# Optimization experiments

Measured on AMD Instinct MI355X. Metric: run time of the kernel, lower is better.

The kernel has to match this reference:

```python
import jax, jax.numpy as jnp
import numpy as np

N_NODES = 50000
N_EDGES = 800000
IN_DIM = 64
HID_DIM = 128
OUT_DIM = 64
BN_EPS = 1e-5


def _glorot(key, shape):
    fan_in, fan_out = shape[0], shape[1]
    lim = (6.0 / (fan_in + fan_out)) ** 0.5
    return jax.random.uniform(key, shape, jnp.float32, -lim, lim)


def setup_inputs() -> dict:
    key = jax.random.key(0)
    ks = jax.random.split(key, 8)
    x = jax.random.normal(ks[0], (N_NODES, IN_DIM), jnp.float32)
    edge_index = jax.random.randint(ks[1], (2, N_EDGES), 0, N_NODES, jnp.int32)
    return {
        "x": x,
        "edge_index": edge_index,
        # SAGEConv1: lin_l (applied to aggregated neighbors, has bias), lin_r (root, no bias)
        "W1l": _glorot(ks[2], (IN_DIM, HID_DIM)),
        "b1": jnp.zeros((HID_DIM,), jnp.float32),
        "W1r": _glorot(ks[3], (IN_DIM, HID_DIM)),
        # BatchNorm1d params
        "gamma": jnp.ones((HID_DIM,), jnp.float32),
        "beta": jnp.zeros((HID_DIM,), jnp.float32),
        # SAGEConv2
        "W2l": _glorot(ks[4], (HID_DIM, OUT_DIM)),
        "b2": jnp.zeros((OUT_DIM,), jnp.float32),
        "W2r": _glorot(ks[5], (HID_DIM, OUT_DIM)),
    }


def _sage_conv(h, src, dst, Wl, b, Wr, deg_inv):
    # mean-aggregate neighbor features per destination node
    agg = jax.ops.segment_sum(h[src], dst, num_segments=N_NODES)  # [N, d]
    agg = agg * deg_inv[:, None]
    return agg @ Wl + b + h @ Wr


def reference(x, edge_index, W1l, b1, W1r, gamma, beta, W2l, b2, W2r):
    src, dst = edge_index[0], edge_index[1]
    deg = jax.ops.segment_sum(jnp.ones((N_EDGES,), jnp.float32), dst,
                              num_segments=N_NODES)
    deg_inv = jnp.where(deg > 0, 1.0 / jnp.maximum(deg, 1.0), 0.0)

    h = _sage_conv(x, src, dst, W1l, b1, W1r, deg_inv)  # [N, hid]
    # BatchNorm1d (training mode: batch stats over nodes, biased variance)
    mu = jnp.mean(h, axis=0)
    var = jnp.mean((h - mu) ** 2, axis=0)
    h = (h - mu) * jax.lax.rsqrt(var + BN_EPS) * gamma + beta
    h = jax.nn.relu(h)
    out = _sage_conv(h, src, dst, W2l, b2, W2r, deg_inv)  # [N, out]
    return out
```

## Files before the change

kernel.cpp:

```cpp
#include <hip/hip_runtime.h>

#define NN 50000
#define NE 800000
#define HID 128
#define OUTD 64
#define NBK 782
#define BWID 64
#define CAP 1264
#define TILE_E 4096
#define XB 3125
#define HB 196

typedef __attribute__((ext_vector_type(8))) short bf16x8;
typedef __attribute__((ext_vector_type(4))) float f32x4;

static __device__ __forceinline__ unsigned short f2bf(float f) {
    unsigned u = __float_as_uint(f);
    unsigned r = (u + 0x7FFFu + ((u >> 16) & 1u)) >> 16;
    return (unsigned short)r;
}
static __device__ __forceinline__ float bflo(unsigned u) { return __uint_as_float(u << 16); }
static __device__ __forceinline__ float bfhi(unsigned u) { return __uint_as_float(u & 0xffff0000u); }

__global__ __launch_bounds__(256) void prep_bin_kernel(
    const float* __restrict__ x, unsigned short* __restrict__ xb,
    const float* __restrict__ W1l, const float* __restrict__ W1r,
    const float* __restrict__ W2l, const float* __restrict__ W2r,
    unsigned short* __restrict__ BT1, unsigned short* __restrict__ BT2,
    const int* __restrict__ src, const int* __restrict__ dst,
    int* __restrict__ gcur, unsigned* __restrict__ pairs)
{
    __shared__ int lcnt[NBK];
    __shared__ int lbase[NBK];
    int blk = blockIdx.x, tid = threadIdx.x;
    if (blk >= HB) {
        int b2 = blk - HB;
        if (b2 < XB) {
            int idx = b2 * 256 + tid;
            int n = idx >> 4, q = idx & 15;
            float4 v = ((const float4*)x)[idx];
            ushort4 o;
            o.x = f2bf(v.x); o.y = f2bf(v.y); o.z = f2bf(v.z); o.w = f2bf(v.w);
            *(ushort4*)(xb + (size_t)n * 64 + q * 4) = o;
        } else {
            int idx = (b2 - XB) * 256 + tid;
            int j = idx >> 7, k = idx & 127;
            float v1 = (k < 64) ? W1l[k * HID + j] : W1r[(k - 64) * HID + j];
            BT1[j * 128 + k] = f2bf(v1);
            float v2 = (j < 64) ? W2l[k * OUTD + j] : W2r[k * OUTD + (j - 64)];
            BT2[j * 128 + k] = f2bf(v2);
        }
        return;
    }
    int e0 = blk * TILE_E;
    for (int i = tid; i < NBK; i += 256) lcnt[i] = 0;
    __syncthreads();
    int s[16], d[16], loc[16];
#pragma unroll
    for (int i = 0; i < 16; i++) {
        int e = e0 + i * 256 + tid;
        if (e < NE) {
            s[i] = __builtin_nontemporal_load(&src[e]);
            d[i] = __builtin_nontemporal_load(&dst[e]);
            loc[i] = atomicAdd(&lcnt[d[i] >> 6], 1);
        }
    }
    __syncthreads();
    for (int b = tid; b < NBK; b += 256)
        lbase[b] = b * CAP + atomicAdd(&gcur[b], lcnt[b]);
    __syncthreads();
#pragma unroll
    for (int i = 0; i < 16; i++) {
        int e = e0 + i * 256 + tid;
        if (e < NE)
            pairs[lbase[d[i] >> 6] + loc[i]] =
                (unsigned)(((d[i] & 63) << 16) | s[i]);
    }
}

__global__ __launch_bounds__(256) void agg_conv1_kernel(
    const unsigned* __restrict__ pairs, const int* __restrict__ gcur,
    const unsigned short* __restrict__ xb, const unsigned short* __restrict__ BT,
    const float* __restrict__ bias, unsigned short* __restrict__ hpreb,
    float* __restrict__ sums, float* __restrict__ sumsq,
    unsigned short* __restrict__ permG, unsigned short* __restrict__ degG,
    unsigned short* __restrict__ startG)
{
    __shared__ int lcnt[BWID];
    __shared__ int startL[BWID];
    __shared__ int degL[BWID];
    __shared__ int lcur[BWID];
    __shared__ __align__(16) unsigned short permL[CAP];
    __shared__ __align__(16) unsigned short aggL[64][64];
    __shared__ float red_s[4][128];
    __shared__ float red_q[4][128];
    int b = blockIdx.x, tid = threadIdx.x;
    int lo = b * CAP;
    int cnt = gcur[b];
    if (tid < BWID) lcnt[tid] = 0;
    __syncthreads();
    for (int i = tid; i < cnt; i += 256)
        atomicAdd(&lcnt[pairs[lo + i] >> 16], 1);
    __syncthreads();
    if (tid < BWID) {
        int v = lcnt[tid];
        int s = v;
#pragma unroll
        for (int off = 1; off < BWID; off <<= 1) {
            int t = __shfl_up(s, off, 64);
            if (tid >= off) s += t;
        }
        startL[tid] = s - v;
        degL[tid] = v;
        lcur[tid] = s - v;
        degG[b * 64 + tid] = (unsigned short)v;
        startG[b * 64 + tid] = (unsigned short)(s - v);
    }
    __syncthreads();
    for (int i = tid; i < cnt; i += 256) {
        unsigned p = pairs[lo + i];
        int pos = atomicAdd(&lcur[p >> 16], 1);
        permL[pos] = (unsigned short)(p & 0xffffu);
    }
    __syncthreads();
    int cu = (cnt + 1) >> 1;
    for (int i = tid; i < cu; i += 256)
        ((unsigned*)(permG + lo))[i] = ((const unsigned*)permL)[i];
    int lane = tid & 63, w = tid >> 6;
    int g = lane >> 3;
    int q = lane & 7;
    const unsigned short* fbase = xb + q * 8;
#pragma unroll
    for (int rnd = 0; rnd < 2; rnd++) {
        int nloc = w * 16 + rnd * 8 + g;
        int rs = startL[nloc];
        int deg = degL[nloc];
        float acc[8];
#pragma unroll
        for (int t = 0; t < 8; t++) acc[t] = 0.f;
        int i = 0;
        for (; i + 3 < deg; i += 4) {
            int s0 = permL[rs + i];
            int s1 = permL[rs + i + 1];
            int s2 = permL[rs + i + 2];
            int s3 = permL[rs + i + 3];
            uint4 v0 = *(const uint4*)(fbase + (size_t)s0 * 64);
            uint4 v1 = *(const uint4*)(fbase + (size_t)s1 * 64);
            uint4 v2 = *(const uint4*)(fbase + (size_t)s2 * 64);
            uint4 v3 = *(const uint4*)(fbase + (size_t)s3 * 64);
            acc[0] += bflo(v0.x); acc[1] += bfhi(v0.x);
            acc[2] += bflo(v0.y); acc[3] += bfhi(v0.y);
            acc[4] += bflo(v0.z); acc[5] += bfhi(v0.z);
            acc[6] += bflo(v0.w); acc[7] += bfhi(v0.w);
            acc[0] += bflo(v1.x); acc[1] += bfhi(v1.x);
            acc[2] += bflo(v1.y); acc[3] += bfhi(v1.y);
            acc[4] += bflo(v1.z); acc[5] += bfhi(v1.z);
            acc[6] += bflo(v1.w); acc[7] += bfhi(v1.w);
            acc[0] += bflo(v2.x); acc[1] += bfhi(v2.x);
            acc[2] += bflo(v2.y); acc[3] += bfhi(v2.y);
            acc[4] += bflo(v2.z); acc[5] += bfhi(v2.z);
            acc[6] += bflo(v2.w); acc[7] += bfhi(v2.w);
            acc[0] += bflo(v3.x); acc[1] += bfhi(v3.x);
            acc[2] += bflo(v3.y); acc[3] += bfhi(v3.y);
            acc[4] += bflo(v3.z); acc[5] += bfhi(v3.z);
            acc[6] += bflo(v3.w); acc[7] += bfhi(v3.w);
        }
        for (; i < deg; i++) {
            int s0 = permL[rs + i];
            uint4 v0 = *(const uint4*)(fbase + (size_t)s0 * 64);
            acc[0] += bflo(v0.x); acc[1] += bfhi(v0.x);
            acc[2] += bflo(v0.y); acc[3] += bfhi(v0.y);
            acc[4] += bflo(v0.z); acc[5] += bfhi(v0.z);
            acc[6] += bflo(v0.w); acc[7] += bfhi(v0.w);
        }
        float inv = (deg > 0) ? (1.0f / (float)deg) : 0.f;
        uint4 o;
        o.x = (unsigned)f2bf(acc[0] * inv) | ((unsigned)f2bf(acc[1] * inv) << 16);
        o.y = (unsigned)f2bf(acc[2] * inv) | ((unsigned)f2bf(acc[3] * inv) << 16);
        o.z = (unsigned)f2bf(acc[4] * inv) | ((unsigned)f2bf(acc[5] * inv) << 16);
        o.w = (unsigned)f2bf(acc[6] * inv) | ((unsigned)f2bf(acc[7] * inv) << 16);
        *(uint4*)&aggL[nloc][q * 8] = o;
    }
    __syncthreads();
    int nl = lane & 15, ko = lane >> 4;
    int jh = w & 1;
    bf16x8 bfr[4][4];
    const unsigned short* bbase = BT + (size_t)(jh * 64 + nl) * 128 + ko * 8;
#pragma unroll
    for (int jg = 0; jg < 4; jg++)
#pragma unroll
        for (int ks = 0; ks < 4; ks++)
            bfr[jg][ks] = *(const bf16x8*)(bbase + jg * 16 * 128 + ks * 32);
    float4 bias4[4];
#pragma unroll
    for (int jg = 0; jg < 4; jg++)
        bias4[jg] = *(const float4*)(bias + jh * 64 + jg * 16 + ko * 4);
    float s_sum[16], s_sq[16];
#pragma unroll
    for (int t = 0; t < 16; t++) { s_sum[t] = 0.f; s_sq[t] = 0.f; }
#pragma unroll
    for (int rnd2 = 0; rnd2 < 2; rnd2++) {
        int t = (w >> 1) + rnd2 * 2;
        int n_g = b * 64 + t * 16 + nl;
        if (n_g < NN) {
            bf16x8 a[4];
#pragma unroll
            for (int ks = 0; ks < 2; ks++)
                a[ks] = *(const bf16x8*)&aggL[t * 16 + nl][ks * 32 + ko * 8];
            const unsigned short* xrow = xb + (size_t)n_g * 64 + ko * 8;
#pragma unroll
            for (int ks = 2; ks < 4; ks++)
                a[ks] = *(const bf16x8*)(xrow + (ks - 2) * 32);
#pragma unroll
            for (int jg = 0; jg < 4; jg++) {
                f32x4 acc = {0.f, 0.f, 0.f, 0.f};
#pragma unroll
                for (int ks = 0; ks < 4; ks++)
                    acc = __builtin_amdgcn_mfma_f32_16x16x32_bf16(bfr[jg][ks], a[ks], acc, 0, 0, 0);
                float v0 = acc[0] + bias4[jg].x;
                float v1 = acc[1] + bias4[jg].y;
                float v2 = acc[2] + bias4[jg].z;
                float v3 = acc[3] + bias4[jg].w;
                s_sum[jg * 4 + 0] += v0; s_sq[jg * 4 + 0] += v0 * v0;
                s_sum[jg * 4 + 1] += v1; s_sq[jg * 4 + 1] += v1 * v1;
                s_sum[jg * 4 + 2] += v2; s_sq[jg * 4 + 2] += v2 * v2;
                s_sum[jg * 4 + 3] += v3; s_sq[jg * 4 + 3] += v3 * v3;
                uint2 pk;
                pk.x = (unsigned)f2bf(v0) | ((unsigned)f2bf(v1) << 16);
                pk.y = (unsigned)f2bf(v2) | ((unsigned)f2bf(v3) << 16);
                *(uint2*)(hpreb + (size_t)n_g * 128 + jh * 64 + jg * 16 + ko * 4) = pk;
            }
        }
    }
    for (int i = tid; i < 512; i += 256) {
        ((float*)red_s)[i] = 0.f;
        ((float*)red_q)[i] = 0.f;
    }
    __syncthreads();
#pragma unroll
    for (int jg = 0; jg < 4; jg++) {
#pragma unroll
        for (int r = 0; r < 4; r++) {
            float v = s_sum[jg * 4 + r];
            v += __shfl_xor(v, 1, 64);
            v += __shfl_xor(v, 2, 64);
            v += __shfl_xor(v, 4, 64);
            v += __shfl_xor(v, 8, 64);
            float w2 = s_sq[jg * 4 + r];
            w2 += __shfl_xor(w2, 1, 64);
            w2 += __shfl_xor(w2, 2, 64);
            w2 += __shfl_xor(w2, 4, 64);
            w2 += __shfl_xor(w2, 8, 64);
            if (nl == 0) {
                red_s[w][jh * 64 + jg * 16 + ko * 4 + r] = v;
                red_q[w][jh * 64 + jg * 16 + ko * 4 + r] = w2;
            }
        }
    }
    __syncthreads();
    if (tid < 128) {
        float v = red_s[0][tid] + red_s[1][tid] + red_s[2][tid] + red_s[3][tid];
        atomicAdd(&sums[tid], v);
    } else {
        int j = tid - 128;
        float v = red_q[0][j] + red_q[1][j] + red_q[2][j] + red_q[3][j];
        atomicAdd(&sumsq[j], v);
    }
}

static __device__ __forceinline__ bf16x8 bnrelu8(uint4 v, const float* sc,
                                                 const float* sh, int j0) {
    float f[8];
    f[0] = bflo(v.x); f[1] = bfhi(v.x);
    f[2] = bflo(v.y); f[3] = bfhi(v.y);
    f[4] = bflo(v.z); f[5] = bfhi(v.z);
    f[6] = bflo(v.w); f[7] = bfhi(v.w);
#pragma unroll
    for (int t = 0; t < 8; t++) {
        float h = f[t] * sc[j0 + t] + sh[j0 + t];
        f[t] = h > 0.f ? h : 0.f;
    }
    unsigned r01 = (unsigned)f2bf(f[0]) | ((unsigned)f2bf(f[1]) << 16);
    unsigned r23 = (unsigned)f2bf(f[2]) | ((unsigned)f2bf(f[3]) << 16);
    unsigned r45 = (unsigned)f2bf(f[4]) | ((unsigned)f2bf(f[5]) << 16);
    unsigned r67 = (unsigned)f2bf(f[6]) | ((unsigned)f2bf(f[7]) << 16);
    uint4 o = make_uint4(r01, r23, r45, r67);
    return *(bf16x8*)&o;
}

__global__ __launch_bounds__(256) void conv2_kernel(
    const unsigned short* __restrict__ A, const unsigned short* __restrict__ BT,
    const float* __restrict__ bias,
    unsigned short* __restrict__ pb, float* __restrict__ outf,
    const float* __restrict__ sums, const float* __restrict__ sumsq,
    const float* __restrict__ gamma, const float* __restrict__ beta)
{
    __shared__ float sc[128], sh[128];
    int tid = threadIdx.x;
    int wid = tid >> 6, lane = tid & 63;
    int nl = lane & 15, ko = lane >> 4;
    if (tid < 128) {
        float inv_n = 1.0f / (float)NN;
        float mu = sums[tid] * inv_n;
        float var = sumsq[tid] * inv_n - mu * mu;
        float s = gamma[tid] * rsqrtf(var + 1e-5f);
        sc[tid] = s;
        sh[tid] = beta[tid] - mu * s;
    }
    __syncthreads();
    int gw = blockIdx.x * 4 + wid;
    int jh = gw & 1;
    int tstride = (gridDim.x * 4) >> 1;
    const int tiles = NN / 16;
    bf16x8 bfr[4][4];
    const unsigned short* bbase = BT + (size_t)(jh * 64 + nl) * 128 + ko * 8;
#pragma unroll
    for (int jg = 0; jg < 4; jg++)
#pragma unroll
        for (int ks = 0; ks < 4; ks++)
            bfr[jg][ks] = *(const bf16x8*)(bbase + jg * 16 * 128 + ks * 32);
    float4 bias4[4];
#pragma unroll
    for (int jg = 0; jg < 4; jg++) {
        if (jh) bias4[jg] = *(const float4*)(bias + jg * 16 + ko * 4);
        else    bias4[jg] = make_float4(0.f, 0.f, 0.f, 0.f);
    }
    int tile = gw >> 1;
    uint4 a[4];
    if (tile < tiles) {
        const unsigned short* arow = A + (size_t)(tile * 16 + nl) * 128 + ko * 8;
#pragma unroll
        for (int ks = 0; ks < 4; ks++) a[ks] = *(const uint4*)(arow + ks * 32);
    }
    while (tile < tiles) {
        int nxt = tile + tstride;
        uint4 an[4];
        if (nxt < tiles) {
            const unsigned short* arow = A + (size_t)(nxt * 16 + nl) * 128 + ko * 8;
#pragma unroll
            for (int ks = 0; ks < 4; ks++) an[ks] = *(const uint4*)(arow + ks * 32);
        }
        bf16x8 af[4];
#pragma unroll
        for (int ks = 0; ks < 4; ks++)
            af[ks] = bnrelu8(a[ks], sc, sh, ks * 32 + ko * 8);
        int n_g = tile * 16 + nl;
#pragma unroll
        for (int jg = 0; jg < 4; jg++) {
            f32x4 acc = {0.f, 0.f, 0.f, 0.f};
#pragma unroll
            for (int ks = 0; ks < 4; ks++)
                acc = __builtin_amdgcn_mfma_f32_16x16x32_bf16(bfr[jg][ks], af[ks], acc, 0, 0, 0);
            float v0 = acc[0] + bias4[jg].x;
            float v1 = acc[1] + bias4[jg].y;
            float v2 = acc[2] + bias4[jg].z;
            float v3 = acc[3] + bias4[jg].w;
            if (jh == 0) {
                uint2 pk;
                pk.x = (unsigned)f2bf(v0) | ((unsigned)f2bf(v1) << 16);
                pk.y = (unsigned)f2bf(v2) | ((unsigned)f2bf(v3) << 16);
                *(uint2*)(pb + (size_t)n_g * 64 + jg * 16 + ko * 4) = pk;
            } else {
                float4 o = make_float4(v0, v1, v2, v3);
                *(float4*)(outf + (size_t)n_g * 64 + jg * 16 + ko * 4) = o;
            }
        }
#pragma unroll
        for (int ks = 0; ks < 4; ks++) a[ks] = an[ks];
        tile = nxt;
    }
}

__global__ __launch_bounds__(256) void agg2_kernel(
    const unsigned short* __restrict__ permG, const int* __restrict__ gcur,
    const unsigned short* __restrict__ degG, const unsigned short* __restrict__ startG,
    const unsigned short* __restrict__ pb, float* __restrict__ out)
{
    __shared__ __align__(16) unsigned short permL[CAP];
    __shared__ int startL[BWID];
    __shared__ int degL[BWID];
    int b = blockIdx.x, tid = threadIdx.x;
    int lo = b * CAP;
    int cnt = gcur[b];
    if (tid < BWID) {
        startL[tid] = startG[b * 64 + tid];
        degL[tid] = degG[b * 64 + tid];
    }
    int cu = (cnt + 1) >> 1;
    for (int i = tid; i < cu; i += 256)
        ((unsigned*)permL)[i] = ((const unsigned*)(permG + lo))[i];
    __syncthreads();
    int lane = tid & 63, w = tid >> 6;
    int g = lane >> 3;
    int q = lane & 7;
    const unsigned short* fbase = pb + q * 8;
#pragma unroll
    for (int rnd = 0; rnd < 2; rnd++) {
        int nloc = w * 16 + rnd * 8 + g;
        int node = b * 64 + nloc;
        int rs = startL[nloc];
        int deg = degL[nloc];
        float acc[8];
#pragma unroll
        for (int t = 0; t < 8; t++) acc[t] = 0.f;
        int i = 0;
        for (; i + 3 < deg; i += 4) {
            int s0 = permL[rs + i];
            int s1 = permL[rs + i + 1];
            int s2 = permL[rs + i + 2];
            int s3 = permL[rs + i + 3];
            uint4 v0 = *(const uint4*)(fbase + (size_t)s0 * 64);
            uint4 v1 = *(const uint4*)(fbase + (size_t)s1 * 64);
            uint4 v2 = *(const uint4*)(fbase + (size_t)s2 * 64);
            uint4 v3 = *(const uint4*)(fbase + (size_t)s3 * 64);
            acc[0] += bflo(v0.x); acc[1] += bfhi(v0.x);
            acc[2] += bflo(v0.y); acc[3] += bfhi(v0.y);
            acc[4] += bflo(v0.z); acc[5] += bfhi(v0.z);
            acc[6] += bflo(v0.w); acc[7] += bfhi(v0.w);
            acc[0] += bflo(v1.x); acc[1] += bfhi(v1.x);
            acc[2] += bflo(v1.y); acc[3] += bfhi(v1.y);
            acc[4] += bflo(v1.z); acc[5] += bfhi(v1.z);
            acc[6] += bflo(v1.w); acc[7] += bfhi(v1.w);
            acc[0] += bflo(v2.x); acc[1] += bfhi(v2.x);
            acc[2] += bflo(v2.y); acc[3] += bfhi(v2.y);
            acc[4] += bflo(v2.z); acc[5] += bfhi(v2.z);
            acc[6] += bflo(v2.w); acc[7] += bfhi(v2.w);
            acc[0] += bflo(v3.x); acc[1] += bfhi(v3.x);
            acc[2] += bflo(v3.y); acc[3] += bfhi(v3.y);
            acc[4] += bflo(v3.z); acc[5] += bfhi(v3.z);
            acc[6] += bflo(v3.w); acc[7] += bfhi(v3.w);
        }
        for (; i < deg; i++) {
            int s0 = permL[rs + i];
            uint4 v0 = *(const uint4*)(fbase + (size_t)s0 * 64);
            acc[0] += bflo(v0.x); acc[1] += bfhi(v0.x);
            acc[2] += bflo(v0.y); acc[3] += bfhi(v0.y);
            acc[4] += bflo(v0.z); acc[5] += bfhi(v0.z);
            acc[6] += bflo(v0.w); acc[7] += bfhi(v0.w);
        }
        if (node < NN) {
            float inv = (deg > 0) ? (1.0f / (float)deg) : 0.f;
            float4* op = (float4*)(out + (size_t)node * 64 + q * 8);
            float4 o0 = op[0], o1 = op[1];
            o0.x += acc[0] * inv; o0.y += acc[1] * inv;
            o0.z += acc[2] * inv; o0.w += acc[3] * inv;
            o1.x += acc[4] * inv; o1.y += acc[5] * inv;
            o1.z += acc[6] * inv; o1.w += acc[7] * inv;
            op[0] = o0; op[1] = o1;
        }
    }
}

extern "C" void kernel_launch(void* const* d_in, const int* in_sizes, int n_in,
                              void* d_out, int out_size, void* d_ws, size_t ws_size,
                              hipStream_t stream) {
    const float* x     = (const float*)d_in[0];
    const int*   ei    = (const int*)d_in[1];
    const float* W1l   = (const float*)d_in[2];
    const float* b1    = (const float*)d_in[3];
    const float* W1r   = (const float*)d_in[4];
    const float* gamma = (const float*)d_in[5];
    const float* beta  = (const float*)d_in[6];
    const float* W2l   = (const float*)d_in[7];
    const float* b2    = (const float*)d_in[8];
    const float* W2r   = (const float*)d_in[9];
    float* out = (float*)d_out;

    char* wsb = (char*)d_ws;
    int*   gcur   = (int*)wsb;
    float* sums   = (float*)(wsb + 4096);
    float* sumsq  = sums + 128;
    unsigned* pairs = (unsigned*)(wsb + 8192);
    unsigned short* permG  = (unsigned short*)((char*)pairs + (size_t)NBK * CAP * 4);
    unsigned short* degG   = permG + (size_t)NBK * CAP;
    unsigned short* startG = degG + (size_t)NBK * 64;
    unsigned short* xb     = startG + (size_t)NBK * 64;
    unsigned short* hpreb  = xb + (size_t)NN * 64;
    unsigned short* pbuf   = hpreb + (size_t)NN * 128;
    unsigned short* BT1    = pbuf + (size_t)NN * 64;
    unsigned short* BT2    = BT1 + 128 * 128;

    const int* srcp = ei;
    const int* dstp = ei + NE;

    hipMemsetAsync(d_ws, 0, 8192, stream);

    prep_bin_kernel<<<HB + XB + 64, 256, 0, stream>>>(x, xb, W1l, W1r, W2l, W2r,
                                                      BT1, BT2, srcp, dstp, gcur, pairs);
    agg_conv1_kernel<<<NBK, 256, 0, stream>>>(pairs, gcur, xb, BT1, b1, hpreb,
                                              sums, sumsq, permG, degG, startG);
    conv2_kernel<<<512, 256, 0, stream>>>(hpreb, BT2, b2, pbuf, out,
                                          sums, sumsq, gamma, beta);
    agg2_kernel<<<NBK, 256, 0, stream>>>(permG, gcur, degG, startG, pbuf, out);
}
```

Baseline: 190.5 us.

## Split each destination bucket across two blocks in both aggregation kernels

Both aggregation kernels now launch two blocks per 64-node destination bucket. Each block handles 32 destination nodes, filtering the bucket's pairs by half, and stores its own permutation slice and count (cntH) for reuse in the second aggregation. The aim is to double block count, giving more parallelism and finer load balance across CUs, and to shrink per-block LDS so more blocks fit per CU. The cost is that each block scans the full bucket's pairs twice. Bucket capacity is enlarged so each half fits in a fixed 704-entry slot, which adds a small overflow risk if one half receives an unusually large share of edges.

Result: no change. 188.0 us (-1.3%).

```diff
diff --git a/kernel.cpp b/kernel.cpp
--- a/kernel.cpp
+++ b/kernel.cpp
@@ -6,7 +6,8 @@
 #define OUTD 64
 #define NBK 782
 #define BWID 64
-#define CAP 1264
+#define CAP 1408
+#define CAPH 704
 #define TILE_E 4096
 #define XB 3125
 #define HB 196
@@ -84,57 +85,68 @@
     const float* __restrict__ bias, unsigned short* __restrict__ hpreb,
     float* __restrict__ sums, float* __restrict__ sumsq,
     unsigned short* __restrict__ permG, unsigned short* __restrict__ degG,
-    unsigned short* __restrict__ startG)
+    unsigned short* __restrict__ startG, unsigned short* __restrict__ cntH)
 {
-    __shared__ int lcnt[BWID];
-    __shared__ int startL[BWID];
-    __shared__ int degL[BWID];
-    __shared__ int lcur[BWID];
-    __shared__ __align__(16) unsigned short permL[CAP];
-    __shared__ __align__(16) unsigned short aggL[64][64];
+    __shared__ int lcnt[32];
+    __shared__ int startL[32];
+    __shared__ int degL[32];
+    __shared__ int lcur[32];
+    __shared__ int cntS;
+    __shared__ __align__(4) unsigned short permL[CAPH];
+    __shared__ __align__(16) unsigned short aggL[32][64];
     __shared__ float red_s[4][128];
     __shared__ float red_q[4][128];
-    int b = blockIdx.x, tid = threadIdx.x;
+    int bh = blockIdx.x;
+    int b = bh >> 1, h = bh & 1;
+    int tid = threadIdx.x;
     int lo = b * CAP;
     int cnt = gcur[b];
-    if (tid < BWID) lcnt[tid] = 0;
-    __syncthreads();
-    for (int i = tid; i < cnt; i += 256)
-        atomicAdd(&lcnt[pairs[lo + i] >> 16], 1);
-    __syncthreads();
-    if (tid < BWID) {
+    int dlo = h * 32;
+    if (tid < 32) lcnt[tid] = 0;
+    __syncthreads();
+    for (int i = tid; i < cnt; i += 256) {
+        int dl = (int)(pairs[lo + i] >> 16) - dlo;
+        if ((dl & ~31) == 0) atomicAdd(&lcnt[dl], 1);
+    }
+    __syncthreads();
+    if (tid < 32) {
         int v = lcnt[tid];
         int s = v;
 #pragma unroll
-        for (int off = 1; off < BWID; off <<= 1) {
+        for (int off = 1; off < 32; off <<= 1) {
             int t = __shfl_up(s, off, 64);
             if (tid >= off) s += t;
         }
         startL[tid] = s - v;
         degL[tid] = v;
         lcur[tid] = s - v;
-        degG[b * 64 + tid] = (unsigned short)v;
-        startG[b * 64 + tid] = (unsigned short)(s - v);
+        degG[b * 64 + dlo + tid] = (unsigned short)v;
+        startG[b * 64 + dlo + tid] = (unsigned short)(s - v);
+        if (tid == 31) { cntH[bh] = (unsigned short)s; cntS = s; }
     }
     __syncthreads();
     for (int i = tid; i < cnt; i += 256) {
         unsigned p = pairs[lo + i];
-        int pos = atomicAdd(&lcur[p >> 16], 1);
-        permL[pos] = (unsigned short)(p & 0xffffu);
-    }
-    __syncthreads();
-    int cu = (cnt + 1) >> 1;
+        int dl = (int)(p >> 16) - dlo;
+        if ((dl & ~31) == 0) {
+            int pos = atomicAdd(&lcur[dl], 1);
+            permL[pos] = (unsigned short)(p & 0xffffu);
+        }
+    }
+    __syncthreads();
+    int cs = cntS;
+    int cu = (cs + 1) >> 1;
+    unsigned* pgbase = (unsigned*)(permG + (size_t)b * CAP + h * CAPH);
     for (int i = tid; i < cu; i += 256)
-        ((unsigned*)(permG + lo))[i] = ((const unsigned*)permL)[i];
+        pgbase[i] = ((const unsigned*)permL)[i];
     int lane = tid & 63, w = tid >> 6;
     int g = lane >> 3;
     int q = lane & 7;
+    int ln = w * 8 + g;
     const unsigned short* fbase = xb + q * 8;
-#pragma unroll
-    for (int rnd = 0; rnd < 2; rnd++) {
-        int nloc = w * 16 + rnd * 8 + g;
-        int rs = startL[nloc];
-        int deg = degL[nloc];
+    {
+        int rs = startL[ln];
+        int deg = degL[ln];
         float acc[8];
 #pragma unroll
         for (int t = 0; t < 8; t++) acc[t] = 0.f;
@@ -179,11 +191,11 @@
         o.y = (unsigned)f2bf(acc[2] * inv) | ((unsigned)f2bf(acc[3] * inv) << 16);
         o.z = (unsigned)f2bf(acc[4] * inv) | ((unsigned)f2bf(acc[5] * inv) << 16);
         o.w = (unsigned)f2bf(acc[6] * inv) | ((unsigned)f2bf(acc[7] * inv) << 16);
-        *(uint4*)&aggL[nloc][q * 8] = o;
+        *(uint4*)&aggL[ln][q * 8] = o;
     }
     __syncthreads();
     int nl = lane & 15, ko = lane >> 4;
-    int jh = w & 1;
+    int jh = w & 1, t = w >> 1;
     bf16x8 bfr[4][4];
     const unsigned short* bbase = BT + (size_t)(jh * 64 + nl) * 128 + ko * 8;
 #pragma unroll
@@ -197,39 +209,35 @@
         bias4[jg] = *(const float4*)(bias + jh * 64 + jg * 16 + ko * 4);
     float s_sum[16], s_sq[16];
 #pragma unroll
-    for (int t = 0; t < 16; t++) { s_sum[t] = 0.f; s_sq[t] = 0.f; }
-#pragma unroll
-    for (int rnd2 = 0; rnd2 < 2; rnd2++) {
-        int t = (w >> 1) + rnd2 * 2;
-        int n_g = b * 64 + t * 16 + nl;
-        if (n_g < NN) {
-            bf16x8 a[4];
-#pragma unroll
-            for (int ks = 0; ks < 2; ks++)
-                a[ks] = *(const bf16x8*)&aggL[t * 16 + nl][ks * 32 + ko * 8];
-            const unsigned short* xrow = xb + (size_t)n_g * 64 + ko * 8;
-#pragma unroll
-            for (int ks = 2; ks < 4; ks++)
-                a[ks] = *(const bf16x8*)(xrow + (ks - 2) * 32);
-#pragma unroll
-            for (int jg = 0; jg < 4; jg++) {
-                f32x4 acc = {0.f, 0.f, 0.f, 0.f};
-#pragma unroll
-                for (int ks = 0; ks < 4; ks++)
-                    acc = __builtin_amdgcn_mfma_f32_16x16x32_bf16(bfr[jg][ks], a[ks], acc, 0, 0, 0);
-                float v0 = acc[0] + bias4[jg].x;
-                float v1 = acc[1] + bias4[jg].y;
-                float v2 = acc[2] + bias4[jg].z;
-                float v3 = acc[3] + bias4[jg].w;
-                s_sum[jg * 4 + 0] += v0; s_sq[jg * 4 + 0] += v0 * v0;
-                s_sum[jg * 4 + 1] += v1; s_sq[jg * 4 + 1] += v1 * v1;
-                s_sum[jg * 4 + 2] += v2; s_sq[jg * 4 + 2] += v2 * v2;
-                s_sum[jg * 4 + 3] += v3; s_sq[jg * 4 + 3] += v3 * v3;
-                uint2 pk;
-                pk.x = (unsigned)f2bf(v0) | ((unsigned)f2bf(v1) << 16);
-                pk.y = (unsigned)f2bf(v2) | ((unsigned)f2bf(v3) << 16);
-                *(uint2*)(hpreb + (size_t)n_g * 128 + jh * 64 + jg * 16 + ko * 4) = pk;
-            }
+    for (int tt = 0; tt < 16; tt++) { s_sum[tt] = 0.f; s_sq[tt] = 0.f; }
+    int n_g = b * 64 + h * 32 + t * 16 + nl;
+    if (n_g < NN) {
+        bf16x8 a[4];
+#pragma unroll
+        for (int ks = 0; ks < 2; ks++)
+            a[ks] = *(const bf16x8*)&aggL[t * 16 + nl][ks * 32 + ko * 8];
+        const unsigned short* xrow = xb + (size_t)n_g * 64 + ko * 8;
+#pragma unroll
+        for (int ks = 2; ks < 4; ks++)
+            a[ks] = *(const bf16x8*)(xrow + (ks - 2) * 32);
+#pragma unroll
+        for (int jg = 0; jg < 4; jg++) {
+            f32x4 acc = {0.f, 0.f, 0.f, 0.f};
+#pragma unroll
+            for (int ks = 0; ks < 4; ks++)
+                acc = __builtin_amdgcn_mfma_f32_16x16x32_bf16(bfr[jg][ks], a[ks], acc, 0, 0, 0);
+            float v0 = acc[0] + bias4[jg].x;
+            float v1 = acc[1] + bias4[jg].y;
+            float v2 = acc[2] + bias4[jg].z;
+            float v3 = acc[3] + bias4[jg].w;
+            s_sum[jg * 4 + 0] += v0; s_sq[jg * 4 + 0] += v0 * v0;
+            s_sum[jg * 4 + 1] += v1; s_sq[jg * 4 + 1] += v1 * v1;
+            s_sum[jg * 4 + 2] += v2; s_sq[jg * 4 + 2] += v2 * v2;
+            s_sum[jg * 4 + 3] += v3; s_sq[jg * 4 + 3] += v3 * v3;
+            uint2 pk;
+            pk.x = (unsigned)f2bf(v0) | ((unsigned)f2bf(v1) << 16);
+            pk.y = (unsigned)f2bf(v2) | ((unsigned)f2bf(v3) << 16);
+            *(uint2*)(hpreb + (size_t)n_g * 128 + jh * 64 + jg * 16 + ko * 4) = pk;
         }
     }
     for (int i = tid; i < 512; i += 256) {
@@ -372,82 +380,80 @@
 }
 
 __global__ __launch_bounds__(256) void agg2_kernel(
-    const unsigned short* __restrict__ permG, const int* __restrict__ gcur,
+    const unsigned short* __restrict__ permG, const unsigned short* __restrict__ cntH,
     const unsigned short* __restrict__ degG, const unsigned short* __restrict__ startG,
     const unsigned short* __restrict__ pb, float* __restrict__ out)
 {
-    __shared__ __align__(16) unsigned short permL[CAP];
-    __shared__ int startL[BWID];
-    __shared__ int degL[BWID];
-    int b = blockIdx.x, tid = threadIdx.x;
-    int lo = b * CAP;
-    int cnt = gcur[b];
-    if (tid < BWID) {
-        startL[tid] = startG[b * 64 + tid];
-        degL[tid] = degG[b * 64 + tid];
-    }
-    int cu = (cnt + 1) >> 1;
+    __shared__ __align__(4) unsigned short permL[CAPH];
+    __shared__ int startL[32];
+    __shared__ int degL[32];
+    int bh = blockIdx.x, b = bh >> 1, h = bh & 1;
+    int tid = threadIdx.x;
+    if (tid < 32) {
+        startL[tid] = startG[b * 64 + h * 32 + tid];
+        degL[tid] = degG[b * 64 + h * 32 + tid];
+    }
+    int cs = cntH[bh];
+    int cu = (cs + 1) >> 1;
+    const unsigned* pgbase = (const unsigned*)(permG + (size_t)b * CAP + h * CAPH);
     for (int i = tid; i < cu; i += 256)
-        ((unsigned*)permL)[i] = ((const unsigned*)(permG + lo))[i];
+        ((unsigned*)permL)[i] = pgbase[i];
     __syncthreads();
     int lane = tid & 63, w = tid >> 6;
     int g = lane >> 3;
     int q = lane & 7;
+    int ln = w * 8 + g;
+    int node = b * 64 + h * 32 + ln;
     const unsigned short* fbase = pb + q * 8;
-#pragma unroll
-    for (int rnd = 0; rnd < 2; rnd++) {
-        int nloc = w * 16 + rnd * 8 + g;
-        int node = b * 64 + nloc;
-        int rs = startL[nloc];
-        int deg = degL[nloc];
-        float acc[8];
-#pragma unroll
-        for (int t = 0; t < 8; t++) acc[t] = 0.f;
-        int i = 0;
-        for (; i + 3 < deg; i += 4) {
-            int s0 = permL[rs + i];
-            int s1 = permL[rs + i + 1];
-            int s2 = permL[rs + i + 2];
-            int s3 = permL[rs + i + 3];
-            uint4 v0 = *(const uint4*)(fbase + (size_t)s0 * 64);
-            uint4 v1 = *(const uint4*)(fbase + (size_t)s1 * 64);
-            uint4 v2 = *(const uint4*)(fbase + (size_t)s2 * 64);
-            uint4 v3 = *(const uint4*)(fbase + (size_t)s3 * 64);
-            acc[0] += bflo(v0.x); acc[1] += bfhi(v0.x);
-            acc[2] += bflo(v0.y); acc[3] += bfhi(v0.y);
-            acc[4] += bflo(v0.z); acc[5] += bfhi(v0.z);
-            acc[6] += bflo(v0.w); acc[7] += bfhi(v0.w);
-            acc[0] += bflo(v1.x); acc[1] += bfhi(v1.x);
-            acc[2] += bflo(v1.y); acc[3] += bfhi(v1.y);
-            acc[4] += bflo(v1.z); acc[5] += bfhi(v1.z);
-            acc[6] += bflo(v1.w); acc[7] += bfhi(v1.w);
-            acc[0] += bflo(v2.x); acc[1] += bfhi(v2.x);
-            acc[2] += bflo(v2.y); acc[3] += bfhi(v2.y);
-            acc[4] += bflo(v2.z); acc[5] += bfhi(v2.z);
-            acc[6] += bflo(v2.w); acc[7] += bfhi(v2.w);
-            acc[0] += bflo(v3.x); acc[1] += bfhi(v3.x);
-            acc[2] += bflo(v3.y); acc[3] += bfhi(v3.y);
-            acc[4] += bflo(v3.z); acc[5] += bfhi(v3.z);
-            acc[6] += bflo(v3.w); acc[7] += bfhi(v3.w);
-        }
-        for (; i < deg; i++) {
-            int s0 = permL[rs + i];
-            uint4 v0 = *(const uint4*)(fbase + (size_t)s0 * 64);
-            acc[0] += bflo(v0.x); acc[1] += bfhi(v0.x);
-            acc[2] += bflo(v0.y); acc[3] += bfhi(v0.y);
-            acc[4] += bflo(v0.z); acc[5] += bfhi(v0.z);
-            acc[6] += bflo(v0.w); acc[7] += bfhi(v0.w);
-        }
-        if (node < NN) {
-            float inv = (deg > 0) ? (1.0f / (float)deg) : 0.f;
-            float4* op = (float4*)(out + (size_t)node * 64 + q * 8);
-            float4 o0 = op[0], o1 = op[1];
-            o0.x += acc[0] * inv; o0.y += acc[1] * inv;
-            o0.z += acc[2] * inv; o0.w += acc[3] * inv;
-            o1.x += acc[4] * inv; o1.y += acc[5] * inv;
-            o1.z += acc[6] * inv; o1.w += acc[7] * inv;
-            op[0] = o0; op[1] = o1;
-        }
+    int rs = startL[ln];
+    int deg = degL[ln];
+    float acc[8];
+#pragma unroll
+    for (int t = 0; t < 8; t++) acc[t] = 0.f;
+    int i = 0;
+    for (; i + 3 < deg; i += 4) {
+        int s0 = permL[rs + i];
+        int s1 = permL[rs + i + 1];
+        int s2 = permL[rs + i + 2];
+        int s3 = permL[rs + i + 3];
+        uint4 v0 = *(const uint4*)(fbase + (size_t)s0 * 64);
+        uint4 v1 = *(const uint4*)(fbase + (size_t)s1 * 64);
+        uint4 v2 = *(const uint4*)(fbase + (size_t)s2 * 64);
+        uint4 v3 = *(const uint4*)(fbase + (size_t)s3 * 64);
+        acc[0] += bflo(v0.x); acc[1] += bfhi(v0.x);
+        acc[2] += bflo(v0.y); acc[3] += bfhi(v0.y);
+        acc[4] += bflo(v0.z); acc[5] += bfhi(v0.z);
+        acc[6] += bflo(v0.w); acc[7] += bfhi(v0.w);
+        acc[0] += bflo(v1.x); acc[1] += bfhi(v1.x);
+        acc[2] += bflo(v1.y); acc[3] += bfhi(v1.y);
+        acc[4] += bflo(v1.z); acc[5] += bfhi(v1.z);
+        acc[6] += bflo(v1.w); acc[7] += bfhi(v1.w);
+        acc[0] += bflo(v2.x); acc[1] += bfhi(v2.x);
+        acc[2] += bflo(v2.y); acc[3] += bfhi(v2.y);
+        acc[4] += bflo(v2.z); acc[5] += bfhi(v2.z);
+        acc[6] += bflo(v2.w); acc[7] += bfhi(v2.w);
+        acc[0] += bflo(v3.x); acc[1] += bfhi(v3.x);
+        acc[2] += bflo(v3.y); acc[3] += bfhi(v3.y);
+        acc[4] += bflo(v3.z); acc[5] += bfhi(v3.z);
+        acc[6] += bflo(v3.w); acc[7] += bfhi(v3.w);
+    }
+    for (; i < deg; i++) {
+        int s0 = permL[rs + i];
+        uint4 v0 = *(const uint4*)(fbase + (size_t)s0 * 64);
+        acc[0] += bflo(v0.x); acc[1] += bfhi(v0.x);
+        acc[2] += bflo(v0.y); acc[3] += bfhi(v0.y);
+        acc[4] += bflo(v0.z); acc[5] += bfhi(v0.z);
+        acc[6] += bflo(v0.w); acc[7] += bfhi(v0.w);
+    }
+    if (node < NN) {
+        float inv = (deg > 0) ? (1.0f / (float)deg) : 0.f;
+        float4* op = (float4*)(out + (size_t)node * 64 + q * 8);
+        float4 o0 = op[0], o1 = op[1];
+        o0.x += acc[0] * inv; o0.y += acc[1] * inv;
+        o0.z += acc[2] * inv; o0.w += acc[3] * inv;
+        o1.x += acc[4] * inv; o1.y += acc[5] * inv;
+        o1.z += acc[6] * inv; o1.w += acc[7] * inv;
+        op[0] = o0; op[1] = o1;
     }
 }
 
@@ -474,7 +480,8 @@
     unsigned short* permG  = (unsigned short*)((char*)pairs + (size_t)NBK * CAP * 4);
     unsigned short* degG   = permG + (size_t)NBK * CAP;
     unsigned short* startG = degG + (size_t)NBK * 64;
-    unsigned short* xb     = startG + (size_t)NBK * 64;
+    unsigned short* cntH   = startG + (size_t)NBK * 64;
+    unsigned short* xb     = cntH + 4096;
     unsigned short* hpreb  = xb + (size_t)NN * 64;
     unsigned short* pbuf   = hpreb + (size_t)NN * 128;
     unsigned short* BT1    = pbuf + (size_t)NN * 64;
@@ -487,9 +494,9 @@
 
     prep_bin_kernel<<<HB + XB + 64, 256, 0, stream>>>(x, xb, W1l, W1r, W2l, W2r,
                                                       BT1, BT2, srcp, dstp, gcur, pairs);
-    agg_conv1_kernel<<<NBK, 256, 0, stream>>>(pairs, gcur, xb, BT1, b1, hpreb,
-                                              sums, sumsq, permG, degG, startG);
+    agg_conv1_kernel<<<NBK * 2, 256, 0, stream>>>(pairs, gcur, xb, BT1, b1, hpreb,
+                                                  sums, sumsq, permG, degG, startG, cntH);
     conv2_kernel<<<512, 256, 0, stream>>>(hpreb, BT2, b2, pbuf, out,
                                           sums, sumsq, gamma, beta);
-    agg2_kernel<<<NBK, 256, 0, stream>>>(permG, gcur, degG, startG, pbuf, out);
-}
+    agg2_kernel<<<NBK * 2, 256, 0, stream>>>(permG, cntH, degG, startG, pbuf, out);
+}
```

## Use 512-thread blocks for aggregation kernels and spread BN stat atomics

Applied to the files above, without the earlier changes.

Doubles the block size of the conv1 aggregation and agg2 kernels so each wave handles one group of destination nodes, dropping the two-round loop. This gives more waves in flight for the latency-bound gathers. BatchNorm sum and sum-of-squares atomics are spread over 8 partial buffers indexed by block, which conv2 then sums, to reduce atomic contention. It also enlarges the per-bucket capacity and pads the aggL shared tile to avoid bank conflicts, at the cost of more shared memory and register pressure per block.

Result: faster. 170.9 us (-10.3%).

```diff
diff --git a/kernel.cpp b/kernel.cpp
--- a/kernel.cpp
+++ b/kernel.cpp
@@ -5,8 +5,7 @@
 #define HID 128
 #define OUTD 64
 #define NBK 782
-#define BWID 64
-#define CAP 1264
+#define CAP 1408
 #define TILE_E 4096
 #define XB 3125
 #define HB 196
@@ -78,35 +77,35 @@
     }
 }
 
-__global__ __launch_bounds__(256) void agg_conv1_kernel(
+__global__ __launch_bounds__(512) void agg_conv1_kernel(
     const unsigned* __restrict__ pairs, const int* __restrict__ gcur,
     const unsigned short* __restrict__ xb, const unsigned short* __restrict__ BT,
     const float* __restrict__ bias, unsigned short* __restrict__ hpreb,
-    float* __restrict__ sums, float* __restrict__ sumsq,
+    float* __restrict__ sums_p, float* __restrict__ sumsq_p,
     unsigned short* __restrict__ permG, unsigned short* __restrict__ degG,
     unsigned short* __restrict__ startG)
 {
-    __shared__ int lcnt[BWID];
-    __shared__ int startL[BWID];
-    __shared__ int degL[BWID];
-    __shared__ int lcur[BWID];
-    __shared__ __align__(16) unsigned short permL[CAP];
-    __shared__ __align__(16) unsigned short aggL[64][64];
+    __shared__ int lcnt[64];
+    __shared__ int startL[64];
+    __shared__ int degL[64];
+    __shared__ int lcur[64];
+    __shared__ __align__(4) unsigned short permL[CAP];
+    __shared__ __align__(16) unsigned short aggL[64][72];
     __shared__ float red_s[4][128];
     __shared__ float red_q[4][128];
     int b = blockIdx.x, tid = threadIdx.x;
     int lo = b * CAP;
     int cnt = gcur[b];
-    if (tid < BWID) lcnt[tid] = 0;
-    __syncthreads();
-    for (int i = tid; i < cnt; i += 256)
+    if (tid < 64) lcnt[tid] = 0;
+    __syncthreads();
+    for (int i = tid; i < cnt; i += 512)
         atomicAdd(&lcnt[pairs[lo + i] >> 16], 1);
     __syncthreads();
-    if (tid < BWID) {
+    if (tid < 64) {
         int v = lcnt[tid];
         int s = v;
 #pragma unroll
-        for (int off = 1; off < BWID; off <<= 1) {
+        for (int off = 1; off < 64; off <<= 1) {
             int t = __shfl_up(s, off, 64);
             if (tid >= off) s += t;
         }
@@ -117,24 +116,24 @@
         startG[b * 64 + tid] = (unsigned short)(s - v);
     }
     __syncthreads();
-    for (int i = tid; i < cnt; i += 256) {
+    for (int i = tid; i < cnt; i += 512) {
         unsigned p = pairs[lo + i];
         int pos = atomicAdd(&lcur[p >> 16], 1);
         permL[pos] = (unsigned short)(p & 0xffffu);
     }
     __syncthreads();
     int cu = (cnt + 1) >> 1;
-    for (int i = tid; i < cu; i += 256)
-        ((unsigned*)(permG + lo))[i] = ((const unsigned*)permL)[i];
+    unsigned* pgb = (unsigned*)(permG + (size_t)b * CAP);
+    for (int i = tid; i < cu; i += 512)
+        pgb[i] = ((const unsigned*)permL)[i];
     int lane = tid & 63, w = tid >> 6;
     int g = lane >> 3;
     int q = lane & 7;
+    int ln = w * 8 + g;
     const unsigned short* fbase = xb + q * 8;
-#pragma unroll
-    for (int rnd = 0; rnd < 2; rnd++) {
-        int nloc = w * 16 + rnd * 8 + g;
-        int rs = startL[nloc];
-        int deg = degL[nloc];
+    {
+        int rs = startL[ln];
+        int deg = degL[ln];
         float acc[8];
 #pragma unroll
         for (int t = 0; t < 8; t++) acc[t] = 0.f;
@@ -179,11 +178,11 @@
         o.y = (unsigned)f2bf(acc[2] * inv) | ((unsigned)f2bf(acc[3] * inv) << 16);
         o.z = (unsigned)f2bf(acc[4] * inv) | ((unsigned)f2bf(acc[5] * inv) << 16);
         o.w = (unsigned)f2bf(acc[6] * inv) | ((unsigned)f2bf(acc[7] * inv) << 16);
-        *(uint4*)&aggL[nloc][q * 8] = o;
+        *(uint4*)&aggL[ln][q * 8] = o;
     }
     __syncthreads();
     int nl = lane & 15, ko = lane >> 4;
-    int jh = w & 1;
+    int jh = w & 1, t = w >> 1;
     bf16x8 bfr[4][4];
     const unsigned short* bbase = BT + (size_t)(jh * 64 + nl) * 128 + ko * 8;
 #pragma unroll
@@ -197,46 +196,37 @@
         bias4[jg] = *(const float4*)(bias + jh * 64 + jg * 16 + ko * 4);
     float s_sum[16], s_sq[16];
 #pragma unroll
-    for (int t = 0; t < 16; t++) { s_sum[t] = 0.f; s_sq[t] = 0.f; }
-#pragma unroll
-    for (int rnd2 = 0; rnd2 < 2; rnd2++) {
-        int t = (w >> 1) + rnd2 * 2;
-        int n_g = b * 64 + t * 16 + nl;
-        if (n_g < NN) {
-            bf16x8 a[4];
-#pragma unroll
-            for (int ks = 0; ks < 2; ks++)
-                a[ks] = *(const bf16x8*)&aggL[t * 16 + nl][ks * 32 + ko * 8];
-            const unsigned short* xrow = xb + (size_t)n_g * 64 + ko * 8;
-#pragma unroll
-            for (int ks = 2; ks < 4; ks++)
-                a[ks] = *(const bf16x8*)(xrow + (ks - 2) * 32);
-#pragma unroll
-            for (int jg = 0; jg < 4; jg++) {
-                f32x4 acc = {0.f, 0.f, 0.f, 0.f};
-#pragma unroll
-                for (int ks = 0; ks < 4; ks++)
-                    acc = __builtin_amdgcn_mfma_f32_16x16x32_bf16(bfr[jg][ks], a[ks], acc, 0, 0, 0);
-                float v0 = acc[0] + bias4[jg].x;
-                float v1 = acc[1] + bias4[jg].y;
-                float v2 = acc[2] + bias4[jg].z;
-                float v3 = acc[3] + bias4[jg].w;
-                s_sum[jg * 4 + 0] += v0; s_sq[jg * 4 + 0] += v0 * v0;
-                s_sum[jg * 4 + 1] += v1; s_sq[jg * 4 + 1] += v1 * v1;
-                s_sum[jg * 4 + 2] += v2; s_sq[jg * 4 + 2] += v2 * v2;
-                s_sum[jg * 4 + 3] += v3; s_sq[jg * 4 + 3] += v3 * v3;
-                uint2 pk;
-                pk.x = (unsigned)f2bf(v0) | ((unsigned)f2bf(v1) << 16);
-                pk.y = (unsigned)f2bf(v2) | ((unsigned)f2bf(v3) << 16);
-                *(uint2*)(hpreb + (size_t)n_g * 128 + jh * 64 + jg * 16 + ko * 4) = pk;
-            }
-        }
-    }
-    for (int i = tid; i < 512; i += 256) {
-        ((float*)red_s)[i] = 0.f;
-        ((float*)red_q)[i] = 0.f;
-    }
-    __syncthreads();
+    for (int tt = 0; tt < 16; tt++) { s_sum[tt] = 0.f; s_sq[tt] = 0.f; }
+    int n_g = b * 64 + t * 16 + nl;
+    if (n_g < NN) {
+        bf16x8 a[4];
+#pragma unroll
+        for (int ks = 0; ks < 2; ks++)
+            a[ks] = *(const bf16x8*)&aggL[t * 16 + nl][ks * 32 + ko * 8];
+        const unsigned short* xrow = xb + (size_t)n_g * 64 + ko * 8;
+#pragma unroll
+        for (int ks = 2; ks < 4; ks++)
+            a[ks] = *(const bf16x8*)(xrow + (ks - 2) * 32);
+#pragma unroll
+        for (int jg = 0; jg < 4; jg++) {
+            f32x4 acc = {0.f, 0.f, 0.f, 0.f};
+#pragma unroll
+            for (int ks = 0; ks < 4; ks++)
+                acc = __builtin_amdgcn_mfma_f32_16x16x32_bf16(bfr[jg][ks], a[ks], acc, 0, 0, 0);
+            float v0 = acc[0] + bias4[jg].x;
+            float v1 = acc[1] + bias4[jg].y;
+            float v2 = acc[2] + bias4[jg].z;
+            float v3 = acc[3] + bias4[jg].w;
+            s_sum[jg * 4 + 0] += v0; s_sq[jg * 4 + 0] += v0 * v0;
+            s_sum[jg * 4 + 1] += v1; s_sq[jg * 4 + 1] += v1 * v1;
+            s_sum[jg * 4 + 2] += v2; s_sq[jg * 4 + 2] += v2 * v2;
+            s_sum[jg * 4 + 3] += v3; s_sq[jg * 4 + 3] += v3 * v3;
+            uint2 pk;
+            pk.x = (unsigned)f2bf(v0) | ((unsigned)f2bf(v1) << 16);
+            pk.y = (unsigned)f2bf(v2) | ((unsigned)f2bf(v3) << 16);
+            *(uint2*)(hpreb + (size_t)n_g * 128 + jh * 64 + jg * 16 + ko * 4) = pk;
+        }
+    }
 #pragma unroll
     for (int jg = 0; jg < 4; jg++) {
 #pragma unroll
@@ -252,19 +242,19 @@
             w2 += __shfl_xor(w2, 4, 64);
             w2 += __shfl_xor(w2, 8, 64);
             if (nl == 0) {
-                red_s[w][jh * 64 + jg * 16 + ko * 4 + r] = v;
-                red_q[w][jh * 64 + jg * 16 + ko * 4 + r] = w2;
+                red_s[t][jh * 64 + jg * 16 + ko * 4 + r] = v;
+                red_q[t][jh * 64 + jg * 16 + ko * 4 + r] = w2;
             }
         }
     }
     __syncthreads();
     if (tid < 128) {
         float v = red_s[0][tid] + red_s[1][tid] + red_s[2][tid] + red_s[3][tid];
-        atomicAdd(&sums[tid], v);
-    } else {
+        atomicAdd(&sums_p[(b & 7) * 128 + tid], v);
+    } else if (tid < 256) {
         int j = tid - 128;
         float v = red_q[0][j] + red_q[1][j] + red_q[2][j] + red_q[3][j];
-        atomicAdd(&sumsq[j], v);
+        atomicAdd(&sumsq_p[(b & 7) * 128 + j], v);
     }
 }
 
@@ -292,7 +282,7 @@
     const unsigned short* __restrict__ A, const unsigned short* __restrict__ BT,
     const float* __restrict__ bias,
     unsigned short* __restrict__ pb, float* __restrict__ outf,
-    const float* __restrict__ sums, const float* __restrict__ sumsq,
+    const float* __restrict__ sums_p, const float* __restrict__ sumsq_p,
     const float* __restrict__ gamma, const float* __restrict__ beta)
 {
     __shared__ float sc[128], sh[128];
@@ -300,12 +290,18 @@
     int wid = tid >> 6, lane = tid & 63;
     int nl = lane & 15, ko = lane >> 4;
     if (tid < 128) {
+        float s = 0.f, qq = 0.f;
+#pragma unroll
+        for (int p = 0; p < 8; p++) {
+            s  += sums_p[p * 128 + tid];
+            qq += sumsq_p[p * 128 + tid];
+        }
         float inv_n = 1.0f / (float)NN;
-        float mu = sums[tid] * inv_n;
-        float var = sumsq[tid] * inv_n - mu * mu;
-        float s = gamma[tid] * rsqrtf(var + 1e-5f);
-        sc[tid] = s;
-        sh[tid] = beta[tid] - mu * s;
+        float mu = s * inv_n;
+        float var = qq * inv_n - mu * mu;
+        float sf = gamma[tid] * rsqrtf(var + 1e-5f);
+        sc[tid] = sf;
+        sh[tid] = beta[tid] - mu * sf;
     }
     __syncthreads();
     int gw = blockIdx.x * 4 + wid;
@@ -371,83 +367,80 @@
     }
 }
 
-__global__ __launch_bounds__(256) void agg2_kernel(
+__global__ __launch_bounds__(512) void agg2_kernel(
     const unsigned short* __restrict__ permG, const int* __restrict__ gcur,
     const unsigned short* __restrict__ degG, const unsigned short* __restrict__ startG,
     const unsigned short* __restrict__ pb, float* __restrict__ out)
 {
-    __shared__ __align__(16) unsigned short permL[CAP];
-    __shared__ int startL[BWID];
-    __shared__ int degL[BWID];
+    __shared__ __align__(4) unsigned short permL[CAP];
+    __shared__ int startL[64];
+    __shared__ int degL[64];
     int b = blockIdx.x, tid = threadIdx.x;
-    int lo = b * CAP;
     int cnt = gcur[b];
-    if (tid < BWID) {
+    if (tid < 64) {
         startL[tid] = startG[b * 64 + tid];
         degL[tid] = degG[b * 64 + tid];
     }
     int cu = (cnt + 1) >> 1;
-    for (int i = tid; i < cu; i += 256)
-        ((unsigned*)permL)[i] = ((const unsigned*)(permG + lo))[i];
+    const unsigned* pgb = (const unsigned*)(permG + (size_t)b * CAP);
+    for (int i = tid; i < cu; i += 512)
+        ((unsigned*)permL)[i] = pgb[i];
     __syncthreads();
     int lane = tid & 63, w = tid >> 6;
     int g = lane >> 3;
     int q = lane & 7;
+    int ln = w * 8 + g;
+    int node = b * 64 + ln;
     const unsigned short* fbase = pb + q * 8;
-#pragma unroll
-    for (int rnd = 0; rnd < 2; rnd++) {
-        int nloc = w * 16 + rnd * 8 + g;
-        int node = b * 64 + nloc;
-        int rs = startL[nloc];
-        int deg = degL[nloc];
-        float acc[8];
-#pragma unroll
-        for (int t = 0; t < 8; t++) acc[t] = 0.f;
-        int i = 0;
-        for (; i + 3 < deg; i += 4) {
-            int s0 = permL[rs + i];
-            int s1 = permL[rs + i + 1];
-            int s2 = permL[rs + i + 2];
-            int s3 = permL[rs + i + 3];
-            uint4 v0 = *(const uint4*)(fbase + (size_t)s0 * 64);
-            uint4 v1 = *(const uint4*)(fbase + (size_t)s1 * 64);
-            uint4 v2 = *(const uint4*)(fbase + (size_t)s2 * 64);
-            uint4 v3 = *(const uint4*)(fbase + (size_t)s3 * 64);
-            acc[0] += bflo(v0.x); acc[1] += bfhi(v0.x);
-            acc[2] += bflo(v0.y); acc[3] += bfhi(v0.y);
-            acc[4] += bflo(v0.z); acc[5] += bfhi(v0.z);
-            acc[6] += bflo(v0.w); acc[7] += bfhi(v0.w);
-            acc[0] += bflo(v1.x); acc[1] += bfhi(v1.x);
-            acc[2] += bflo(v1.y); acc[3] += bfhi(v1.y);
-            acc[4] += bflo(v1.z); acc[5] += bfhi(v1.z);
-            acc[6] += bflo(v1.w); acc[7] += bfhi(v1.w);
-            acc[0] += bflo(v2.x); acc[1] += bfhi(v2.x);
-            acc[2] += bflo(v2.y); acc[3] += bfhi(v2.y);
-            acc[4] += bflo(v2.z); acc[5] += bfhi(v2.z);
-            acc[6] += bflo(v2.w); acc[7] += bfhi(v2.w);
-            acc[0] += bflo(v3.x); acc[1] += bfhi(v3.x);
-            acc[2] += bflo(v3.y); acc[3] += bfhi(v3.y);
-            acc[4] += bflo(v3.z); acc[5] += bfhi(v3.z);
-            acc[6] += bflo(v3.w); acc[7] += bfhi(v3.w);
-        }
-        for (; i < deg; i++) {
-            int s0 = permL[rs + i];
-            uint4 v0 = *(const uint4*)(fbase + (size_t)s0 * 64);
-            acc[0] += bflo(v0.x); acc[1] += bfhi(v0.x);
-            acc[2] += bflo(v0.y); acc[3] += bfhi(v0.y);
-            acc[4] += bflo(v0.z); acc[5] += bfhi(v0.z);
-            acc[6] += bflo(v0.w); acc[7] += bfhi(v0.w);
-        }
-        if (node < NN) {
-            float inv = (deg > 0) ? (1.0f / (float)deg) : 0.f;
-            float4* op = (float4*)(out + (size_t)node * 64 + q * 8);
-            float4 o0 = op[0], o1 = op[1];
-            o0.x += acc[0] * inv; o0.y += acc[1] * inv;
-            o0.z += acc[2] * inv; o0.w += acc[3] * inv;
-            o1.x += acc[4] * inv; o1.y += acc[5] * inv;
-            o1.z += acc[6] * inv; o1.w += acc[7] * inv;
-            op[0] = o0; op[1] = o1;
-        }
+    int rs = startL[ln];
+    int deg = degL[ln];
+    float acc[8];
+#pragma unroll
+    for (int t = 0; t < 8; t++) acc[t] = 0.f;
+    int i = 0;
+    for (; i + 3 < deg; i += 4) {
+        int s0 = permL[rs + i];
+        int s1 = permL[rs + i + 1];
+        int s2 = permL[rs + i + 2];
+        int s3 = permL[rs + i + 3];
+        uint4 v0 = *(const uint4*)(fbase + (size_t)s0 * 64);
+        uint4 v1 = *(const uint4*)(fbase + (size_t)s1 * 64);
+        uint4 v2 = *(const uint4*)(fbase + (size_t)s2 * 64);
+        uint4 v3 = *(const uint4*)(fbase + (size_t)s3 * 64);
+        acc[0] += bflo(v0.x); acc[1] += bfhi(v0.x);
+        acc[2] += bflo(v0.y); acc[3] += bfhi(v0.y);
+        acc[4] += bflo(v0.z); acc[5] += bfhi(v0.z);
+        acc[6] += bflo(v0.w); acc[7] += bfhi(v0.w);
+        acc[0] += bflo(v1.x); acc[1] += bfhi(v1.x);
+        acc[2] += bflo(v1.y); acc[3] += bfhi(v1.y);
+        acc[4] += bflo(v1.z); acc[5] += bfhi(v1.z);
+        acc[6] += bflo(v1.w); acc[7] += bfhi(v1.w);
+        acc[0] += bflo(v2.x); acc[1] += bfhi(v2.x);
+        acc[2] += bflo(v2.y); acc[3] += bfhi(v2.y);
+        acc[4] += bflo(v2.z); acc[5] += bfhi(v2.z);
+        acc[6] += bflo(v2.w); acc[7] += bfhi(v2.w);
+        acc[0] += bflo(v3.x); acc[1] += bfhi(v3.x);
+        acc[2] += bflo(v3.y); acc[3] += bfhi(v3.y);
+        acc[4] += bflo(v3.z); acc[5] += bfhi(v3.z);
+        acc[6] += bflo(v3.w); acc[7] += bfhi(v3.w);
+    }
+    for (; i < deg; i++) {
+        int s0 = permL[rs + i];
+        uint4 v0 = *(const uint4*)(fbase + (size_t)s0 * 64);
+        acc[0] += bflo(v0.x); acc[1] += bfhi(v0.x);
+        acc[2] += bflo(v0.y); acc[3] += bfhi(v0.y);
+        acc[4] += bflo(v0.z); acc[5] += bfhi(v0.z);
+        acc[6] += bflo(v0.w); acc[7] += bfhi(v0.w);
+    }
+    if (node < NN) {
+        float inv = (deg > 0) ? (1.0f / (float)deg) : 0.f;
+        float4* op = (float4*)(out + (size_t)node * 64 + q * 8);
+        float4 o0 = op[0], o1 = op[1];
+        o0.x += acc[0] * inv; o0.y += acc[1] * inv;
+        o0.z += acc[2] * inv; o0.w += acc[3] * inv;
+        o1.x += acc[4] * inv; o1.y += acc[5] * inv;
+        o1.z += acc[6] * inv; o1.w += acc[7] * inv;
+        op[0] = o0; op[1] = o1;
     }
 }
 
@@ -467,10 +460,10 @@
     float* out = (float*)d_out;
 
     char* wsb = (char*)d_ws;
-    int*   gcur   = (int*)wsb;
-    float* sums   = (float*)(wsb + 4096);
-    float* sumsq  = sums + 128;
-    unsigned* pairs = (unsigned*)(wsb + 8192);
+    int*   gcur    = (int*)wsb;
+    float* sums_p  = (float*)(wsb + 4096);
+    float* sumsq_p = (float*)(wsb + 8192);
+    unsigned* pairs = (unsigned*)(wsb + 12288);
     unsigned short* permG  = (unsigned short*)((char*)pairs + (size_t)NBK * CAP * 4);
     unsigned short* degG   = permG + (size_t)NBK * CAP;
     unsigned short* startG = degG + (size_t)NBK * 64;
@@ -483,13 +476,13 @@
     const int* srcp = ei;
     const int* dstp = ei + NE;
 
-    hipMemsetAsync(d_ws, 0, 8192, stream);
+    hipMemsetAsync(d_ws, 0, 12288, stream);
 
     prep_bin_kernel<<<HB + XB + 64, 256, 0, stream>>>(x, xb, W1l, W1r, W2l, W2r,
                                                       BT1, BT2, srcp, dstp, gcur, pairs);
-    agg_conv1_kernel<<<NBK, 256, 0, stream>>>(pairs, gcur, xb, BT1, b1, hpreb,
-                                              sums, sumsq, permG, degG, startG);
+    agg_conv1_kernel<<<NBK, 512, 0, stream>>>(pairs, gcur, xb, BT1, b1, hpreb,
+                                              sums_p, sumsq_p, permG, degG, startG);
     conv2_kernel<<<512, 256, 0, stream>>>(hpreb, BT2, b2, pbuf, out,
-                                          sums, sumsq, gamma, beta);
-    agg2_kernel<<<NBK, 256, 0, stream>>>(permG, gcur, degG, startG, pbuf, out);
-}
+                                          sums_p, sumsq_p, gamma, beta);
+    agg2_kernel<<<NBK, 512, 0, stream>>>(permG, gcur, degG, startG, pbuf, out);
+}
```
